# Performance work log

Hardware: AMD Instinct MI355X
Metric: run time of the kernel (lower is better)

Reference implementation:

```python
import jax, jax.numpy as jnp
import numpy as np

SLOPE = 0.01   # nn.LeakyReLU default negative_slope
EPS = 1e-8     # nn.CosineSimilarity default eps


def leaky_relu(x):
    return jnp.where(x >= 0, x, SLOPE * x)


def node_conv(x, w, P):
    # x: [B,N,F] (N % P == 0), w: [P,F] -> [B, N//P, F]
    B, N, F = x.shape
    xg = x.reshape(B, N // P, P, F)
    return jnp.einsum('bspf,pf->bsf', xg, w)


def attn_pool(x, w, b, P):
    # GraphAttentionPooling: per window of P nodes, softmax(W x + b) over the
    # window, then attention-weighted sum.  x: [B,N,F] -> [B, N//P, F]
    B, N, F = x.shape
    xg = x.reshape(B, N // P, P, F)
    logits = jnp.einsum('bspf,f->bsp', xg, w) + b  # b: [1] broadcasts
    att = jax.nn.softmax(logits, axis=-1)
    return jnp.einsum('bspf,bsp->bsf', xg, att)


def get_adjacent(pooled):
    # Faithful to the original (buggy) triple loop: every off-diagonal entry
    # ends up overwritten by a zero, and A[i,i]=cos(v_i,v_i) only when 2i<S.
    # Then A += I and A <- D^{-1/2} A D^{-1/2} with D = column sums.
    B, S, F = pooled.shape
    nrm = jnp.maximum(jnp.linalg.norm(pooled, axis=-1), EPS)     # [B,S]
    cos_self = jnp.sum(pooled * pooled, axis=-1) / (nrm * nrm)    # [B,S]
    mask = (2 * jnp.arange(S) < S).astype(pooled.dtype)           # [S]
    diag = cos_self * mask + 1.0                                  # + identity
    A = jax.vmap(jnp.diag)(diag)                                  # [B,S,S]
    d = jnp.sum(A, axis=1)                                        # [B,S]
    dinv = 1.0 / jnp.sqrt(d)
    return dinv[:, :, None] * A * dinv[:, None, :]


def setup_inputs() -> dict:
    key = jax.random.key(0)
    ks = jax.random.split(key, 11)
    B, N, F, HID, NCLASS, P = 64, 512, 2048, 1100, 512, 4
    s1 = 1.0 / np.sqrt(F)
    s2 = 1.0 / np.sqrt(HID)
    return {
        'x': jax.random.normal(ks[0], (B, N, F), dtype=jnp.float32),
        'conv1_w': jax.random.uniform(ks[1], (P, F), jnp.float32, -s1, s1),
        'pool1_w': jax.random.uniform(ks[2], (F,), jnp.float32, -s1, s1),
        'pool1_b': jax.random.uniform(ks[3], (1,), jnp.float32, -s1, s1),
        'prop1_W': jax.random.normal(ks[4], (F, HID), jnp.float32) * s1,
        'prop1_B': jax.random.normal(ks[5], (HID,), jnp.float32) * 0.01,
        'conv2_w': jax.random.uniform(ks[6], (P, HID), jnp.float32, -s2, s2),
        'pool2_w': jax.random.uniform(ks[7], (HID,), jnp.float32, -s2, s2),
        'pool2_b': jax.random.uniform(ks[8], (1,), jnp.float32, -s2, s2),
        'prop2_W': jax.random.normal(ks[9], (HID, NCLASS), jnp.float32) * s2,
        'prop2_B': jax.random.normal(ks[10], (NCLASS,), jnp.float32) * 0.01,
        'pooling_size': 4,
    }


def reference(x, conv1_w, pool1_w, pool1_b, prop1_W, prop1_B,
              conv2_w, pool2_w, pool2_b, prop2_W, prop2_B, pooling_size):
    P = pooling_size
    # stage 1
    pooled1 = attn_pool(x, pool1_w, pool1_b, P)      # [B,S,F]
    h = node_conv(x, conv1_w, P)                      # [B,S,F]
    adj1 = get_adjacent(pooled1)                      # [B,S,S]
    h = jnp.einsum('bij,bjf->bif', adj1, h) @ prop1_W + prop1_B
    h = leaky_relu(h)                                 # [B,S,1100]
    # stage 2
    pooled2 = attn_pool(h, pool2_w, pool2_b, P)       # [B,S2,1100]
    h2 = node_conv(h, conv2_w, P)                     # [B,S2,1100]
    adj2 = get_adjacent(pooled2)                      # [B,S2,S2]
    out = jnp.einsum('bij,bjf->bif', adj2, h2) @ prop2_W + prop2_B
    return leaky_relu(out)                            # [B,S2,nclass]
```

## Files before the change

### kernel.cpp

```cpp
#include <hip/hip_runtime.h>
#include <cstdint>
#include <cstddef>


using u16 = unsigned short;
using u32 = unsigned int;
using floatx4 = __attribute__((ext_vector_type(4))) float;
using shortx8 = __attribute__((ext_vector_type(8))) short;

#define OUT_MODE 1

__device__ __forceinline__ float bf_lo(u32 u) { return __uint_as_float(u << 16); }
__device__ __forceinline__ float bf_hi(u32 u) { return __uint_as_float(u & 0xffff0000u); }
__device__ __forceinline__ float bf2f(u16 s) { return __uint_as_float(((u32)s) << 16); }
__device__ __forceinline__ u16 f2bf(float f) {
  u32 u = __float_as_uint(f);
  u += 0x7fffu + ((u >> 16) & 1u);
  return (u16)(u >> 16);
}

__device__ __forceinline__ float ld_elem(const void* b, size_t i, int isf32) {
  return isf32 ? ((const float*)b)[i] : bf2f(((const u16*)b)[i]);
}
__device__ __forceinline__ void ld8(const void* b, size_t i, int isf32, float* o) {
  if (isf32) {
    const float* p = (const float*)b + i;
    float4 a = *(const float4*)p, c = *(const float4*)(p + 4);
    o[0]=a.x; o[1]=a.y; o[2]=a.z; o[3]=a.w; o[4]=c.x; o[5]=c.y; o[6]=c.z; o[7]=c.w;
  } else {
    const u16* p = (const u16*)b + i;
    uint2 a = *(const uint2*)p, c = *(const uint2*)(p + 4);
    o[0]=bf_lo(a.x); o[1]=bf_hi(a.x); o[2]=bf_lo(a.y); o[3]=bf_hi(a.y);
    o[4]=bf_lo(c.x); o[5]=bf_hi(c.x); o[6]=bf_lo(c.y); o[7]=bf_hi(c.y);
  }
}

#define GLDS16(gp, lp) __builtin_amdgcn_global_load_lds( \
    (const __attribute__((address_space(1))) void*)(gp), \
    (__attribute__((address_space(3))) void*)(lp), 16, 0, 0)

__global__ __launch_bounds__(256) void dtype_probe(const u32* __restrict__ x,
                                                   int* __restrict__ flag) {
  __shared__ int cnt[256];
  int t = threadIdx.x, c = 0;
  for (int i = t; i < 1024; i += 256) {
    u32 e = (x[i] >> 7) & 0xFFu;
    c += (e >= 110u && e <= 134u) ? 1 : 0;
  }
  cnt[t] = c;
  __syncthreads();
  for (int s = 128; s > 0; s >>= 1) {
    if (t < s) cnt[t] += cnt[t + s];
    __syncthreads();
  }
  if (t == 0) *flag = (cnt[0] < 512) ? 1 : 0;
}

__global__ __launch_bounds__(256) void transpose_bf16(
    const void* __restrict__ W, u16* __restrict__ Wt,
    int K, int N, int Kpad, const int* __restrict__ dflag, int wmode)
{
  int wf = (wmode == 2) ? *dflag : wmode;
  __shared__ float tile[64][65];
  int k0 = blockIdx.x * 64, n0 = blockIdx.y * 64;
  int t = threadIdx.x;
  int a = t & 63, b4 = t >> 6;
  for (int kk = b4; kk < 64; kk += 4) {
    int gk = k0 + kk, gn = n0 + a;
    tile[kk][a] = (gk < K && gn < N) ? ld_elem(W, (size_t)gk * N + gn, wf) : 0.f;
  }
  __syncthreads();
  for (int nn = b4; nn < 64; nn += 4) {
    Wt[(size_t)(n0 + nn) * Kpad + (size_t)(k0 + a)] = f2bf(tile[a][nn]);
  }
}

__global__ __launch_bounds__(256) void nodeconv_x(
    const void* __restrict__ X, const void* __restrict__ Wc,
    u16* __restrict__ XC, int K, int mbase,
    const int* __restrict__ dflag, int xmode, int wmode)
{
  int fl = (xmode == 2 || wmode == 2) ? *dflag : 0;
  int xf = (xmode == 2) ? fl : xmode;
  int wf = (wmode == 2) ? fl : wmode;
  int m = blockIdx.x, t = threadIdx.x;
  size_t xb = ((size_t)(mbase + m) * 4) * (size_t)K + (size_t)t * 8;
  float a[8] = {0.f, 0.f, 0.f, 0.f, 0.f, 0.f, 0.f, 0.f};
#pragma unroll
  for (int p = 0; p < 4; ++p) {
    float xv[8], wv[8];
    ld8(X, xb + (size_t)p * K, xf, xv);
    ld8(Wc, (size_t)p * K + (size_t)t * 8, wf, wv);
#pragma unroll
    for (int j = 0; j < 8; ++j) a[j] += xv[j] * wv[j];
  }
  u32 o0 = (u32)f2bf(a[0]) | ((u32)f2bf(a[1]) << 16);
  u32 o1 = (u32)f2bf(a[2]) | ((u32)f2bf(a[3]) << 16);
  u32 o2 = (u32)f2bf(a[4]) | ((u32)f2bf(a[5]) << 16);
  u32 o3 = (u32)f2bf(a[6]) | ((u32)f2bf(a[7]) << 16);
  uint4 ov; ov.x = o0; ov.y = o1; ov.z = o2; ov.w = o3;
  *(uint4*)&XC[(size_t)m * K + (size_t)t * 8] = ov;
}

template <int BM, int BN, int EPI>
__global__ __launch_bounds__(256) void gemm_bf16(
    const u16* __restrict__ A, int lda,
    const u16* __restrict__ Bt, int ldb,
    const void* __restrict__ bias, const void* __restrict__ w2,
    void* __restrict__ C, int ldc,
    int Nn, int K, int mout0,
    const int* __restrict__ dflag, int wmode, int of32m)
{
  constexpr int WTM = BM / 2, WTN = BN / 2;
  constexpr int MI = WTM / 16, NI = WTN / 16;
  constexpr int AO = (BM * 4) / 256, BO = (BN * 4) / 256;
  __shared__ alignas(16) u16 As[BM * 32];
  __shared__ alignas(16) u16 Bs[BN * 32];

  int wf = (wmode == 2) ? *dflag : wmode;
  int tid = threadIdx.x, lane = tid & 63, wave = tid >> 6;
  int m0 = blockIdx.y * BM, n0 = blockIdx.x * BN;
  int wrow = (wave >> 1) * WTM, wcol = (wave & 1) * WTN;
  int quad = lane >> 4, lm = lane & 15;

  const u16* asrc[AO];
  const u16* bsrc[BO];
#pragma unroll
  for (int o = 0; o < AO; ++o) {
    int idx = o * 256 + tid;
    asrc[o] = A + (size_t)(m0 + (idx % BM)) * lda + (idx / BM) * 8;
  }
#pragma unroll
  for (int o = 0; o < BO; ++o) {
    int idx = o * 256 + tid;
    bsrc[o] = Bt + (size_t)(n0 + (idx % BN)) * ldb + (idx / BN) * 8;
  }

  floatx4 acc[MI][NI] = {};
  int kiters = K >> 5;
  for (int it = 0; it < kiters; ++it) {
    int k0 = it * 32;
#pragma unroll
    for (int o = 0; o < AO; ++o)
      GLDS16(asrc[o] + k0, &As[(o * 256 + wave * 64) * 8]);
#pragma unroll
    for (int o = 0; o < BO; ++o)
      GLDS16(bsrc[o] + k0, &Bs[(o * 256 + wave * 64) * 8]);
    __syncthreads();

    shortx8 av[MI], bv[NI];
#pragma unroll
    for (int mi = 0; mi < MI; ++mi)
      av[mi] = *(const shortx8*)&As[(size_t)(quad * BM + wrow + mi * 16 + lm) * 8];
#pragma unroll
    for (int ni = 0; ni < NI; ++ni)
      bv[ni] = *(const shortx8*)&Bs[(size_t)(quad * BN + wcol + ni * 16 + lm) * 8];
#pragma unroll
    for (int mi = 0; mi < MI; ++mi)
#pragma unroll
      for (int ni = 0; ni < NI; ++ni)
        acc[mi][ni] = __builtin_amdgcn_mfma_f32_16x16x32_bf16(av[mi], bv[ni], acc[mi][ni], 0, 0, 0);
    __syncthreads();
  }

#pragma unroll
  for (int ni = 0; ni < NI; ++ni) {
    int gn = n0 + wcol + ni * 16 + lm;
    float bb = (gn < Nn) ? ld_elem(bias, gn, wf) : 0.f;
    if (EPI == 1) {
      float wv[4];
#pragma unroll
      for (int r = 0; r < 4; ++r)
        wv[r] = (gn < Nn) ? ld_elem(w2, (size_t)r * Nn + gn, wf) : 0.f;
#pragma unroll
      for (int mi = 0; mi < MI; ++mi) {
        float h2 = 0.f;
#pragma unroll
        for (int r = 0; r < 4; ++r) {
          float v = acc[mi][ni][r] + bb;
          v = (v >= 0.f) ? v : 0.01f * v;
          h2 += v * wv[r];
        }
        int s = (mout0 + m0 + wrow + mi * 16 + quad * 4) >> 2;
        ((u16*)C)[(size_t)s * ldc + gn] = f2bf(h2);
      }
    } else {
      if (gn < Nn) {
#pragma unroll
        for (int mi = 0; mi < MI; ++mi) {
#pragma unroll
          for (int r = 0; r < 4; ++r) {
            int gm = mout0 + m0 + wrow + mi * 16 + quad * 4 + r;
            float v = acc[mi][ni][r] + bb;
            v = (v >= 0.f) ? v : 0.01f * v;
            size_t ci = (size_t)gm * ldc + gn;
            if (of32m) ((float*)C)[ci] = v;
            else       ((u16*)C)[ci]   = f2bf(v);
          }
        }
      }
    }
  }
}

extern "C" void kernel_launch(void* const* d_in, const int* in_sizes, int n_in,
                              void* d_out, int out_size, void* d_ws, size_t ws_size,
                              hipStream_t stream) {
  const void* x  = d_in[0];
  const void* w1 = d_in[1];
  const void* W1 = d_in[4];
  const void* b1 = d_in[5];
  const void* w2 = d_in[6];
  const void* W2 = d_in[9];
  const void* b2 = d_in[10];

  char* ws = (char*)d_ws;
  int* dflag = (int*)ws;
  u16* W1t = (u16*)(ws + 256);
  u16* W2t = (u16*)(ws + 256 + 4718592);
  u16* H2  = (u16*)(ws + 256 + 4718592 + 1179648);
  const size_t fixed = 256 + 4718592 + 1179648 + 4718592;
  u16* XC = (u16*)(ws + fixed);

  size_t rem = (ws_size > fixed) ? ws_size - fixed : 0;
  size_t cmax = rem / (2048 * 2);
  int CM = (cmax > 8192) ? 8192 : (int)cmax;
  CM &= ~127;
  if (CM < 128) CM = 128;

  dtype_probe<<<1, 256, 0, stream>>>((const u32*)x, dflag);
  transpose_bf16<<<dim3(32, 18), 256, 0, stream>>>(W1, W1t, 2048, 1100, 2048, dflag, 2);
  transpose_bf16<<<dim3(18, 8), 256, 0, stream>>>(W2, W2t, 1100, 512, 1152, dflag, 2);

  for (int mb = 0; mb < 8192; mb += CM) {
    int cm = 8192 - mb; if (cm > CM) cm = CM;
    nodeconv_x<<<cm, 256, 0, stream>>>(x, w1, XC, 2048, mb, dflag, 2, 2);
    gemm_bf16<128, 128, 1><<<dim3(9, cm / 128), 256, 0, stream>>>(
        XC, 2048, W1t, 2048, b1, w2, H2, 1152, 1100, 2048, mb, dflag, 2, 0);
  }
  gemm_bf16<64, 64, 0><<<dim3(8, 32), 256, 0, stream>>>(
      H2, 1152, W2t, 1152, b2, nullptr, d_out, 512, 512, 1152, 0, dflag, 2, OUT_MODE);
}
```

Measured before the change: 552.5 us.

## Double-buffer GEMM LDS tiles, remap blocks per XCD, fuse weight transposes

The GEMM now double-buffers its A/B LDS tiles, so the global-to-LDS loads for the next K step are issued before the current step's MFMAs. This removes one barrier per iteration and overlaps memory with compute. Workgroup IDs are also remapped so that consecutive tiles land on the same XCD, which should improve L2 reuse. The two weight-transpose launches are merged into one kernel. LDS use doubles, which may lower occupancy for the 128x128 tile.

```diff
diff --git a/kernel.cpp b/kernel.cpp
--- a/kernel.cpp
+++ b/kernel.cpp
@@ -56,13 +56,23 @@
   if (t == 0) *flag = (cnt[0] < 512) ? 1 : 0;
 }
 
-__global__ __launch_bounds__(256) void transpose_bf16(
-    const void* __restrict__ W, u16* __restrict__ Wt,
-    int K, int N, int Kpad, const int* __restrict__ dflag, int wmode)
+__global__ __launch_bounds__(256) void transpose2_bf16(
+    const void* __restrict__ W1, u16* __restrict__ W1t,
+    const void* __restrict__ W2, u16* __restrict__ W2t,
+    const int* __restrict__ dflag)
 {
-  int wf = (wmode == 2) ? *dflag : wmode;
+  int wf = *dflag;
   __shared__ float tile[64][65];
-  int k0 = blockIdx.x * 64, n0 = blockIdx.y * 64;
+  int id = blockIdx.x;
+  const void* W; u16* Wt; int K, N, Kpad, k0, n0;
+  if (id < 576) {
+    W = W1; Wt = W1t; K = 2048; N = 1100; Kpad = 2048;
+    k0 = (id % 32) * 64; n0 = (id / 32) * 64;
+  } else {
+    id -= 576;
+    W = W2; Wt = W2t; K = 1100; N = 512; Kpad = 1152;
+    k0 = (id % 18) * 64; n0 = (id / 18) * 64;
+  }
   int t = threadIdx.x;
   int a = t & 63, b4 = t >> 6;
   for (int kk = b4; kk < 64; kk += 4) {
@@ -114,12 +124,21 @@
   constexpr int WTM = BM / 2, WTN = BN / 2;
   constexpr int MI = WTM / 16, NI = WTN / 16;
   constexpr int AO = (BM * 4) / 256, BO = (BN * 4) / 256;
-  __shared__ alignas(16) u16 As[BM * 32];
-  __shared__ alignas(16) u16 Bs[BN * 32];
+  __shared__ alignas(16) u16 As[2][BM * 32];
+  __shared__ alignas(16) u16 Bs[2][BN * 32];
 
   int wf = (wmode == 2) ? *dflag : wmode;
   int tid = threadIdx.x, lane = tid & 63, wave = tid >> 6;
-  int m0 = blockIdx.y * BM, n0 = blockIdx.x * BN;
+
+  int nx = gridDim.x, ny = gridDim.y;
+  int lin = blockIdx.y * nx + blockIdx.x;
+  int nwg = nx * ny;
+  int q = nwg >> 3, r = nwg & 7;
+  int xcd = lin & 7, wi = lin >> 3;
+  int g = (xcd < r ? xcd * (q + 1) : r * (q + 1) + (xcd - r) * q) + wi;
+  int bx = g / ny, by = g - bx * ny;
+
+  int m0 = by * BM, n0 = bx * BN;
   int wrow = (wave >> 1) * WTM, wcol = (wave & 1) * WTN;
   int quad = lane >> 4, lm = lane & 15;
 
@@ -136,31 +155,40 @@
     bsrc[o] = Bt + (size_t)(n0 + (idx % BN)) * ldb + (idx / BN) * 8;
   }
 
+  auto STAGE = [&](int buf, int it) {
+    int k0 = it << 5;
+#pragma unroll
+    for (int o = 0; o < AO; ++o)
+      GLDS16(asrc[o] + k0, &As[buf][(o * 256 + wave * 64) * 8]);
+#pragma unroll
+    for (int o = 0; o < BO; ++o)
+      GLDS16(bsrc[o] + k0, &Bs[buf][(o * 256 + wave * 64) * 8]);
+  };
+
   floatx4 acc[MI][NI] = {};
   int kiters = K >> 5;
+
+  STAGE(0, 0);
+  __syncthreads();
+
   for (int it = 0; it < kiters; ++it) {
-    int k0 = it * 32;
-#pragma unroll
-    for (int o = 0; o < AO; ++o)
-      GLDS16(asrc[o] + k0, &As[(o * 256 + wave * 64) * 8]);
-#pragma unroll
-    for (int o = 0; o < BO; ++o)
-      GLDS16(bsrc[o] + k0, &Bs[(o * 256 + wave * 64) * 8]);
-    __syncthreads();
+    int cur = it & 1;
+    if (it + 1 < kiters) STAGE(cur ^ 1, it + 1);
 
     shortx8 av[MI], bv[NI];
 #pragma unroll
     for (int mi = 0; mi < MI; ++mi)
-      av[mi] = *(const shortx8*)&As[(size_t)(quad * BM + wrow + mi * 16 + lm) * 8];
+      av[mi] = *(const shortx8*)&As[cur][(size_t)(quad * BM + wrow + mi * 16 + lm) * 8];
 #pragma unroll
     for (int ni = 0; ni < NI; ++ni)
-      bv[ni] = *(const shortx8*)&Bs[(size_t)(quad * BN + wcol + ni * 16 + lm) * 8];
+      bv[ni] = *(const shortx8*)&Bs[cur][(size_t)(quad * BN + wcol + ni * 16 + lm) * 8];
 #pragma unroll
     for (int mi = 0; mi < MI; ++mi)
 #pragma unroll
       for (int ni = 0; ni < NI; ++ni)
         acc[mi][ni] = __builtin_amdgcn_mfma_f32_16x16x32_bf16(av[mi], bv[ni], acc[mi][ni], 0, 0, 0);
-    __syncthreads();
+
+    if (it + 1 < kiters) __syncthreads();
   }
 
 #pragma unroll
@@ -229,8 +257,7 @@
   if (CM < 128) CM = 128;
 
   dtype_probe<<<1, 256, 0, stream>>>((const u32*)x, dflag);
-  transpose_bf16<<<dim3(32, 18), 256, 0, stream>>>(W1, W1t, 2048, 1100, 2048, dflag, 2);
-  transpose_bf16<<<dim3(18, 8), 256, 0, stream>>>(W2, W2t, 1100, 512, 1152, dflag, 2);
+  transpose2_bf16<<<720, 256, 0, stream>>>(W1, W1t, W2, W2t, dflag);
 
   for (int mb = 0; mb < 8192; mb += CM) {
     int cm = 8192 - mb; if (cm > CM) cm = CM;
```

Result: faster. 540.2 us (-2.2%).
